# Performance work log

Measured on AMD Instinct MI355X. Metric: run time of the kernel, lower is better.

## Reference

```python
import jax, jax.numpy as jnp
import numpy as np

HIDDEN = 2048
N_HEADS = 32
N_KV = 8
HEAD_DIM = HIDDEN // N_HEADS
SEQ = 2048
BATCH = 1
THETA = 10000.0
EPS = 1e-5


def _layernorm(x, g, b):
    mu = jnp.mean(x, axis=-1, keepdims=True)
    var = jnp.var(x, axis=-1, keepdims=True)
    return (x - mu) * jax.lax.rsqrt(var + EPS) * g + b


def _rope_tables(seq_len, dim, theta):
    inv_freq = 1.0 / (theta ** (jnp.arange(0, dim, 2, dtype=jnp.float32) / dim))
    t = jnp.arange(seq_len, dtype=jnp.float32)
    freqs = jnp.einsum('i,j->ij', t, inv_freq)          # [S, D/2]
    emb = jnp.concatenate([freqs, freqs], axis=-1)       # [S, D]
    return jnp.cos(emb), jnp.sin(emb)


def _rotate_half(x):
    x1, x2 = jnp.split(x, 2, axis=-1)
    return jnp.concatenate([-x2, x1], axis=-1)


def setup_inputs() -> dict:
    key = jax.random.key(0)
    ks = jax.random.split(key, 10)
    s = 0.02
    return {
        'x':   jax.random.normal(ks[0], (BATCH, SEQ, HIDDEN), jnp.float32),
        'Wq':  jax.random.normal(ks[1], (HIDDEN, HIDDEN), jnp.float32) * s,
        'bq':  jnp.zeros((HIDDEN,), jnp.float32),
        'Wk':  jax.random.normal(ks[2], (HIDDEN, N_KV * HEAD_DIM), jnp.float32) * s,
        'bk':  jnp.zeros((N_KV * HEAD_DIM,), jnp.float32),
        'Wv':  jax.random.normal(ks[3], (HIDDEN, N_KV * HEAD_DIM), jnp.float32) * s,
        'bv':  jnp.zeros((N_KV * HEAD_DIM,), jnp.float32),
        'Wo':  jax.random.normal(ks[4], (HIDDEN, HIDDEN), jnp.float32) * s,
        'bo':  jnp.zeros((HIDDEN,), jnp.float32),
        'q_g': jnp.ones((HEAD_DIM,), jnp.float32),
        'q_b': jnp.zeros((HEAD_DIM,), jnp.float32),
        'k_g': jnp.ones((HEAD_DIM,), jnp.float32),
        'k_b': jnp.zeros((HEAD_DIM,), jnp.float32),
    }


def reference(x, Wq, bq, Wk, bk, Wv, bv, Wo, bo, q_g, q_b, k_g, k_b):
    B, S, H = x.shape
    n_rep = N_HEADS // N_KV
    # projections
    q = (x @ Wq + bq).reshape(B, S, N_HEADS, HEAD_DIM).transpose(0, 2, 1, 3)  # [B,Hq,S,D]
    k = (x @ Wk + bk).reshape(B, S, N_KV, HEAD_DIM).transpose(0, 2, 1, 3)     # [B,Hkv,S,D]
    v = (x @ Wv + bv).reshape(B, S, N_KV, HEAD_DIM).transpose(0, 2, 1, 3)
    # per-head QK layernorm
    q = _layernorm(q, q_g, q_b)
    k = _layernorm(k, k_g, k_b)
    # RoPE
    cos, sin = _rope_tables(S, HEAD_DIM, THETA)  # [S, D]
    q = q * cos + _rotate_half(q) * sin
    k = k * cos + _rotate_half(k) * sin
    # GQA attention without materializing repeated k/v:
    # repeat_interleave groups adjacent q-heads per kv head -> reshape q to [B,Hkv,rep,S,D]
    qg = q.reshape(B, N_KV, n_rep, S, HEAD_DIM)
    scores = jnp.einsum('bgrqd,bgkd->bgrqk', qg, k) / jnp.sqrt(jnp.float32(HEAD_DIM))
    attn = jax.nn.softmax(scores, axis=-1)
    out = jnp.einsum('bgrqk,bgkd->bgrqd', attn, v)  # [B,Hkv,rep,S,D]
    out = out.reshape(B, N_HEADS, S, HEAD_DIM).transpose(0, 2, 1, 3).reshape(B, S, H)
    return out @ Wo + bo
```

## Files before the change

### kernel.cpp

```cpp
#include <hip/hip_runtime.h>
#include <hip/hip_bf16.h>
#include <stdint.h>

#define S_LEN 2048
#define HID   2048
#define NH    32
#define NKV   8
#define HD    64

typedef __attribute__((ext_vector_type(8))) short bf16x8;
typedef __attribute__((ext_vector_type(4))) float f32x4;
typedef __attribute__((ext_vector_type(16))) float f32x16;

__device__ __forceinline__ short f2bf(float f) {
  __hip_bfloat16 h = __float2bfloat16(f);
  return __builtin_bit_cast(short, h);
}
__device__ __forceinline__ float bf2f(short s) {
  unsigned u = ((unsigned)(unsigned short)s) << 16;
  return __builtin_bit_cast(float, u);
}
__device__ __forceinline__ int cvt_pk_bf16(float lo, float hi) {
  int r;
  asm("v_cvt_pk_bf16_f32 %0, %1, %2" : "=v"(r) : "v"(lo), "v"(hi));
  return r;
}

__global__ void cast_bf16_kernel(const float* __restrict__ in, short* __restrict__ out, int n4) {
  int i = blockIdx.x * blockDim.x + threadIdx.x;
  if (i < n4) {
    float4 v = reinterpret_cast<const float4*>(in)[i];
    short4 o;
    o.x = f2bf(v.x); o.y = f2bf(v.y); o.z = f2bf(v.z); o.w = f2bf(v.w);
    reinterpret_cast<short4*>(out)[i] = o;
  }
}

__global__ void transpose_cast_kernel(const float* __restrict__ in, short* __restrict__ out,
                                      int K, int N) {
  __shared__ float tile[64][65];
  const int k0 = blockIdx.x * 64;
  const int n0 = blockIdx.y * 64;
  const int tn = threadIdx.x & 63;
  const int t4 = threadIdx.x >> 6;
#pragma unroll
  for (int i = 0; i < 16; i++)
    tile[t4 + i * 4][tn] = in[(size_t)(k0 + t4 + i * 4) * N + n0 + tn];
  __syncthreads();
#pragma unroll
  for (int i = 0; i < 16; i++)
    out[(size_t)(n0 + t4 + i * 4) * K + k0 + tn] = f2bf(tile[tn][t4 + i * 4]);
}

__global__ void concat_bias_kernel(const float* __restrict__ bq, const float* __restrict__ bk,
                                   const float* __restrict__ bv, float* __restrict__ out) {
  int i = blockIdx.x * blockDim.x + threadIdx.x;
  if (i < 3072) {
    float v = (i < 2048) ? bq[i] : (i < 2560 ? bk[i - 2048] : bv[i - 2560]);
    out[i] = v;
  }
}

__global__ void rope_table_kernel(float* __restrict__ ctab, float* __restrict__ stab) {
  int i = blockIdx.x * blockDim.x + threadIdx.x;
  if (i < S_LEN * 32) {
    int t = i >> 5, j = i & 31;
    float ang = (float)t * powf(10000.0f, -(float)j / 32.0f);
    ctab[i] = cosf(ang);
    stab[i] = sinf(ang);
  }
}

template <int F32OUT>
__global__ __launch_bounds__(256, 3) void gemm_v2_kernel(
    const short* __restrict__ A, const short* __restrict__ Bt,
    const float* __restrict__ bias, void* __restrict__ Cv,
    int N, int K) {
  __shared__ short Als[2][64 * 64];
  __shared__ short Bls[2][128 * 64];
  const int tid = threadIdx.x;
  const int l = tid & 63, w = tid >> 6;
  const int lg = l >> 4, lc = l & 15;
  const int wr = w >> 1, wc = w & 1;

  const int nwg = gridDim.x;
  const int cpx = nwg >> 3;
  const int swz = (blockIdx.x & 7) * cpx + (blockIdx.x >> 3);
  const int m0 = (swz & 31) << 6;
  const int n0 = (swz >> 5) << 7;

  const int NT = K >> 6;
  const f32x4 zero4 = {0.f, 0.f, 0.f, 0.f};
  f32x4 acc[2][4];
#pragma unroll
  for (int i = 0; i < 2; i++)
#pragma unroll
    for (int j = 0; j < 4; j++) acc[i][j] = zero4;

  const int lrow = l >> 3;
  const int lcol = (l & 7) << 3;

  auto stage = [&](int buf, int kt) {
    const int kofs = kt << 6;
#pragma unroll
    for (int i = 0; i < 2; i++) {
      const short* gsrc = A + (size_t)(m0 + i * 32 + (w << 3) + lrow) * K + kofs + lcol;
      __builtin_amdgcn_global_load_lds(
          (const __attribute__((address_space(1))) unsigned*)gsrc,
          (__attribute__((address_space(3))) unsigned*)(&Als[buf][(i * 32 + (w << 3)) << 6]),
          16, 0, 0);
    }
#pragma unroll
    for (int i = 0; i < 4; i++) {
      const short* gsrc = Bt + (size_t)(n0 + i * 32 + (w << 3) + lrow) * K + kofs + lcol;
      __builtin_amdgcn_global_load_lds(
          (const __attribute__((address_space(1))) unsigned*)gsrc,
          (__attribute__((address_space(3))) unsigned*)(&Bls[buf][(i * 32 + (w << 3)) << 6]),
          16, 0, 0);
    }
  };

  stage(0, 0);
  int cur = 0;
  for (int kt = 0; kt < NT; kt++) {
    __syncthreads();
    if (kt + 1 < NT) stage(cur ^ 1, kt + 1);
    const char* AB = reinterpret_cast<const char*>(Als[cur]);
    const char* BB = reinterpret_cast<const char*>(Bls[cur]);
#pragma unroll
    for (int ks = 0; ks < 2; ks++) {
      bf16x8 af[2], bfr[4];
#pragma unroll
      for (int mi = 0; mi < 2; mi++)
        af[mi] = *reinterpret_cast<const bf16x8*>(
            AB + (wr * 32 + mi * 16 + lc) * 128 + ks * 64 + lg * 16);
#pragma unroll
      for (int nf = 0; nf < 4; nf++)
        bfr[nf] = *reinterpret_cast<const bf16x8*>(
            BB + (wc * 64 + nf * 16 + lc) * 128 + ks * 64 + lg * 16);
#pragma unroll
      for (int mi = 0; mi < 2; mi++)
#pragma unroll
        for (int nf = 0; nf < 4; nf++)
          acc[mi][nf] = __builtin_amdgcn_mfma_f32_16x16x32_bf16(af[mi], bfr[nf], acc[mi][nf], 0, 0, 0);
    }
    cur ^= 1;
  }

#pragma unroll
  for (int mi = 0; mi < 2; mi++) {
#pragma unroll
    for (int nf = 0; nf < 4; nf++) {
      int col = n0 + wc * 64 + nf * 16 + lc;
      float bv = bias[col];
#pragma unroll
      for (int r = 0; r < 4; r++) {
        int rowg = m0 + wr * 32 + mi * 16 + lg * 4 + r;
        float v = acc[mi][nf][r] + bv;
        if (F32OUT)
          reinterpret_cast<float*>(Cv)[(size_t)rowg * N + col] = v;
        else
          reinterpret_cast<short*>(Cv)[(size_t)rowg * N + col] = f2bf(v);
      }
    }
  }
}

__global__ void ln_rope_kernel(const short* __restrict__ In, int instride, int nh_shift,
                               const float* __restrict__ gam, const float* __restrict__ bet,
                               const float* __restrict__ ctab, const float* __restrict__ stab,
                               float scale, short* __restrict__ Out) {
  const int lane = threadIdx.x & 63;
  const int nh = 1 << nh_shift;
  const int nrows = S_LEN << nh_shift;
  int row = (blockIdx.x * blockDim.x + threadIdx.x) >> 6;
  const int step = (gridDim.x * blockDim.x) >> 6;
  const float g = gam[lane], b = bet[lane];
  for (; row < nrows; row += step) {
    const int t = row >> nh_shift;
    const int h = row & (nh - 1);
    float x = bf2f(In[(size_t)t * instride + h * HD + lane]);
    float s = x;
#pragma unroll
    for (int m = 32; m >= 1; m >>= 1) s += __shfl_xor(s, m);
    const float mu = s * (1.0f / 64.0f);
    float d = x - mu;
    float v2 = d * d;
#pragma unroll
    for (int m = 32; m >= 1; m >>= 1) v2 += __shfl_xor(v2, m);
    const float var = v2 * (1.0f / 64.0f);
    float y = d * rsqrtf(var + 1e-5f) * g + b;
    float part = __shfl_xor(y, 32);
    const float c = ctab[t * 32 + (lane & 31)];
    const float sn = stab[t * 32 + (lane & 31)];
    float o = (lane < 32) ? (y * c - part * sn) : (y * c + part * sn);
    Out[((size_t)h * S_LEN + t) * HD + lane] = f2bf(o * scale);
  }
}

__global__ void v_transpose_kernel(const short* __restrict__ In, short* __restrict__ Vt) {
  __shared__ short tile[64][66];
  const int g = blockIdx.x;
  const int t0 = blockIdx.y * 64;
  const int lane = threadIdx.x & 63, w = threadIdx.x >> 6;
#pragma unroll
  for (int i = 0; i < 16; i++) {
    int r = i * 4 + w;
    tile[r][lane] = In[(size_t)(t0 + r) * 3072 + g * 64 + lane];
  }
  __syncthreads();
#pragma unroll
  for (int i = 0; i < 16; i++) {
    int d = i * 4 + w;
    Vt[((size_t)g * 64 + d) * 2048 + t0 + lane] = tile[lane][d];
  }
}

__global__ __launch_bounds__(256, 2) void attn_kernel(
    const short* __restrict__ Q, const short* __restrict__ Kk,
    const short* __restrict__ Vt, short* __restrict__ AO) {
  __shared__ short Kls[64 * 64];
  __shared__ short Vls[64 * 64];
  const int tid = threadIdx.x;
  const int l = tid & 63;
  const int w = tid >> 6;
  const int q31 = l & 31;
  const int h = l >> 5;

  const int v = (blockIdx.x & 7) * 32 + (blockIdx.x >> 3);
  const int g = v >> 5;
  const int within = v & 31;
  const int head = (g << 2) + (within >> 3);
  const int q0 = (within & 7) * 256 + w * 64;

  bf16x8 qf[2][4];
#pragma unroll
  for (int qb = 0; qb < 2; qb++) {
    const short* qbp = Q + ((size_t)head * S_LEN + q0 + qb * 32 + q31) * HD;
#pragma unroll
    for (int ks = 0; ks < 4; ks++)
      qf[qb][ks] = *reinterpret_cast<const bf16x8*>(qbp + ks * 16 + h * 8);
  }

  f32x16 oacc[2][2];
#pragma unroll
  for (int qb = 0; qb < 2; qb++)
#pragma unroll
    for (int df = 0; df < 2; df++)
#pragma unroll
      for (int r = 0; r < 16; r++) oacc[qb][df][r] = 0.f;
  float l_run[2] = {0.f, 0.f};

  const int srow = tid >> 3;
  const int kb = (tid & 7) << 4;
  const int kbs = kb ^ ((srow & 7) << 4);
  int4 kr[2], vr[2];
  auto stage_load = [&](int kt) {
#pragma unroll
    for (int c = 0; c < 2; c++) {
      int row = c * 32 + srow;
      kr[c] = *reinterpret_cast<const int4*>(Kk + ((size_t)g * S_LEN + kt * 64 + row) * HD + (kb >> 1));
      vr[c] = *reinterpret_cast<const int4*>(Vt + ((size_t)g * HD + row) * S_LEN + kt * 64 + (kb >> 1));
    }
  };
  stage_load(0);

  const int swz = (l & 7) << 4;
  const char* KB = reinterpret_cast<const char*>(Kls);
  const char* VB = reinterpret_cast<const char*>(Vls);

  for (int kt = 0; kt < S_LEN / 64; kt++) {
    __syncthreads();
#pragma unroll
    for (int c = 0; c < 2; c++) {
      int row = c * 32 + srow;
      *reinterpret_cast<int4*>(reinterpret_cast<char*>(Kls) + row * 128 + kbs) = kr[c];
      *reinterpret_cast<int4*>(reinterpret_cast<char*>(Vls) + row * 128 + kbs) = vr[c];
    }
    if (kt + 1 < S_LEN / 64) stage_load(kt + 1);
    __syncthreads();

    f32x16 sc0[2], sc1[2];
#pragma unroll
    for (int i = 0; i < 16; i++) { sc0[0][i] = 0.f; sc0[1][i] = 0.f; sc1[0][i] = 0.f; sc1[1][i] = 0.f; }
    __builtin_amdgcn_s_setprio(1);
#pragma unroll
    for (int ks = 0; ks < 4; ks++) {
#pragma unroll
      for (int kc = 0; kc < 2; kc++) {
        int row = kc * 32 + q31;
        bf16x8 kf = *reinterpret_cast<const bf16x8*>(KB + row * 128 + ((ks * 32 + h * 16) ^ swz));
        sc0[kc] = __builtin_amdgcn_mfma_f32_32x32x16_bf16(kf, qf[0][ks], sc0[kc], 0, 0, 0);
        sc1[kc] = __builtin_amdgcn_mfma_f32_32x32x16_bf16(kf, qf[1][ks], sc1[kc], 0, 0, 0);
      }
    }
    __builtin_amdgcn_s_setprio(0);

    bf16x8 pa[2][4];
#pragma unroll
    for (int qb = 0; qb < 2; qb++) {
      f32x16* sc = (qb == 0) ? sc0 : sc1;
      float ps = 0.f;
#pragma unroll
      for (int kc = 0; kc < 2; kc++)
#pragma unroll
        for (int r = 0; r < 16; r++) {
          float p = __builtin_exp2f(sc[kc][r] - 12.0f);
          sc[kc][r] = p;
          ps += p;
        }
      ps += __shfl_xor(ps, 32);
      l_run[qb] += ps;

#pragma unroll
      for (int c = 0; c < 4; c++) {
        const int b0 = (c & 1) * 8;
        int wa = cvt_pk_bf16(sc[c >> 1][b0 + 0], sc[c >> 1][b0 + 1]);
        int wb = cvt_pk_bf16(sc[c >> 1][b0 + 4], sc[c >> 1][b0 + 5]);
        asm volatile("v_permlane32_swap_b32 %0, %1" : "+v"(wa), "+v"(wb));
        int wc2 = cvt_pk_bf16(sc[c >> 1][b0 + 2], sc[c >> 1][b0 + 3]);
        int wd = cvt_pk_bf16(sc[c >> 1][b0 + 6], sc[c >> 1][b0 + 7]);
        asm volatile("v_permlane32_swap_b32 %0, %1" : "+v"(wc2), "+v"(wd));
        int4 pw;
        pw.x = wa; pw.y = wc2; pw.z = wb; pw.w = wd;
        pa[qb][c] = __builtin_bit_cast(bf16x8, pw);
      }
    }

    __builtin_amdgcn_s_setprio(1);
#pragma unroll
    for (int df = 0; df < 2; df++) {
#pragma unroll
      for (int c = 0; c < 4; c++) {
        int row = df * 32 + q31;
        bf16x8 vf = *reinterpret_cast<const bf16x8*>(VB + row * 128 + ((c * 32 + h * 16) ^ swz));
        oacc[0][df] = __builtin_amdgcn_mfma_f32_32x32x16_bf16(vf, pa[0][c], oacc[0][df], 0, 0, 0);
        oacc[1][df] = __builtin_amdgcn_mfma_f32_32x32x16_bf16(vf, pa[1][c], oacc[1][df], 0, 0, 0);
      }
    }
    __builtin_amdgcn_s_setprio(0);
  }

#pragma unroll
  for (int qb = 0; qb < 2; qb++) {
    float inv = 1.0f / l_run[qb];
    short* aob = AO + (size_t)(q0 + qb * 32 + q31) * HID + head * HD;
#pragma unroll
    for (int df = 0; df < 2; df++) {
#pragma unroll
      for (int rq = 0; rq < 4; rq++) {
        int v0 = cvt_pk_bf16(oacc[qb][df][rq * 4 + 0] * inv, oacc[qb][df][rq * 4 + 1] * inv);
        int v1 = cvt_pk_bf16(oacc[qb][df][rq * 4 + 2] * inv, oacc[qb][df][rq * 4 + 3] * inv);
        int2 st;
        st.x = v0; st.y = v1;
        *reinterpret_cast<int2*>(aob + df * 32 + rq * 8 + h * 4) = st;
      }
    }
  }
}

extern "C" void kernel_launch(void* const* d_in, const int* in_sizes, int n_in,
                              void* d_out, int out_size, void* d_ws, size_t ws_size,
                              hipStream_t stream) {
  const float* x  = (const float*)d_in[0];
  const float* Wq = (const float*)d_in[1];
  const float* bq = (const float*)d_in[2];
  const float* Wk = (const float*)d_in[3];
  const float* bk = (const float*)d_in[4];
  const float* Wv = (const float*)d_in[5];
  const float* bv = (const float*)d_in[6];
  const float* Wo = (const float*)d_in[7];
  const float* bo = (const float*)d_in[8];
  const float* qg = (const float*)d_in[9];
  const float* qb = (const float*)d_in[10];
  const float* kg = (const float*)d_in[11];
  const float* kb2 = (const float*)d_in[12];
  float* out = (float*)d_out;

  char* ws = (char*)d_ws;
  size_t off = 0;
  auto alloc = [&](size_t bytes) {
    void* p = ws + off;
    off += (bytes + 255) & ~(size_t)255;
    return p;
  };
  short* xb    = (short*)alloc((size_t)2048 * 2048 * 2);
  short* Wqkvt = (short*)alloc((size_t)3072 * 2048 * 2);
  short* Wot   = (short*)alloc((size_t)2048 * 2048 * 2);
  short* QKVp  = (short*)alloc((size_t)2048 * 3072 * 2);
  short* Qr    = (short*)alloc((size_t)NH * 2048 * 64 * 2);
  short* Kr    = (short*)alloc((size_t)NKV * 2048 * 64 * 2);
  short* Vt    = (short*)alloc((size_t)NKV * 64 * 2048 * 2);
  short* AO    = (short*)alloc((size_t)2048 * 2048 * 2);
  float* ctab  = (float*)alloc((size_t)2048 * 32 * 4);
  float* stab  = (float*)alloc((size_t)2048 * 32 * 4);
  float* bqkv  = (float*)alloc((size_t)3072 * 4);

  cast_bf16_kernel<<<(2048 * 2048 / 4 + 255) / 256, 256, 0, stream>>>(x, xb, 2048 * 2048 / 4);
  transpose_cast_kernel<<<dim3(32, 32), 256, 0, stream>>>(Wq, Wqkvt, 2048, 2048);
  transpose_cast_kernel<<<dim3(32, 8), 256, 0, stream>>>(Wk, Wqkvt + (size_t)2048 * 2048, 2048, 512);
  transpose_cast_kernel<<<dim3(32, 8), 256, 0, stream>>>(Wv, Wqkvt + (size_t)2560 * 2048, 2048, 512);
  transpose_cast_kernel<<<dim3(32, 32), 256, 0, stream>>>(Wo, Wot, 2048, 2048);
  concat_bias_kernel<<<12, 256, 0, stream>>>(bq, bk, bv, bqkv);
  rope_table_kernel<<<256, 256, 0, stream>>>(ctab, stab);

  gemm_v2_kernel<0><<<768, 256, 0, stream>>>(xb, Wqkvt, bqkv, QKVp, 3072, 2048);

  ln_rope_kernel<<<512, 256, 0, stream>>>(QKVp, 3072, 5, qg, qb, ctab, stab, 0.125f * 1.44269504089f, Qr);
  ln_rope_kernel<<<256, 256, 0, stream>>>(QKVp + 2048, 3072, 3, kg, kb2, ctab, stab, 1.0f, Kr);
  v_transpose_kernel<<<dim3(8, 32), 256, 0, stream>>>(QKVp + 2560, Vt);

  attn_kernel<<<256, 256, 0, stream>>>(Qr, Kr, Vt, AO);

  gemm_v2_kernel<1><<<512, 256, 0, stream>>>(AO, Wot, bo, out, 2048, 2048);
}
```

Before: 344.6 us.

## Split attention KV range in two and merge partial outputs in combine kernel

The attention grid doubles from 256 to 512 blocks, and each block handles half of the key sequence. Each block writes an unnormalized bf16 partial output plus its row sums. A new combine kernel adds the two partials and divides by the summed normalizers. The goal is to fill two blocks per CU for better latency hiding. The costs are an extra launch, extra memory traffic for the partials, and some bf16 rounding of unnormalized sums. The split is valid only because the softmax keeps no running max.

```diff
diff --git a/kernel.cpp b/kernel.cpp
--- a/kernel.cpp
+++ b/kernel.cpp
@@ -218,7 +218,8 @@
 
 __global__ __launch_bounds__(256, 2) void attn_kernel(
     const short* __restrict__ Q, const short* __restrict__ Kk,
-    const short* __restrict__ Vt, short* __restrict__ AO) {
+    const short* __restrict__ Vt, short* __restrict__ Op0,
+    short* __restrict__ Op1, float* __restrict__ lpart) {
   __shared__ short Kls[64 * 64];
   __shared__ short Vls[64 * 64];
   const int tid = threadIdx.x;
@@ -227,11 +228,17 @@
   const int q31 = l & 31;
   const int h = l >> 5;
 
-  const int v = (blockIdx.x & 7) * 32 + (blockIdx.x >> 3);
+  const int bid = blockIdx.x;
+  const int sp = bid >> 8;
+  const int id8 = bid & 255;
+  const int v = (id8 & 7) * 32 + (id8 >> 3);
   const int g = v >> 5;
   const int within = v & 31;
   const int head = (g << 2) + (within >> 3);
   const int q0 = (within & 7) * 256 + w * 64;
+
+  short* __restrict__ Op = sp ? Op1 : Op0;
+  float* __restrict__ lp = lpart + sp * (NH * S_LEN);
 
   bf16x8 qf[2][4];
 #pragma unroll
@@ -263,13 +270,15 @@
       vr[c] = *reinterpret_cast<const int4*>(Vt + ((size_t)g * HD + row) * S_LEN + kt * 64 + (kb >> 1));
     }
   };
-  stage_load(0);
+
+  const int kt0 = sp << 4, kt1 = kt0 + 16;
+  stage_load(kt0);
 
   const int swz = (l & 7) << 4;
   const char* KB = reinterpret_cast<const char*>(Kls);
   const char* VB = reinterpret_cast<const char*>(Vls);
 
-  for (int kt = 0; kt < S_LEN / 64; kt++) {
+  for (int kt = kt0; kt < kt1; kt++) {
     __syncthreads();
 #pragma unroll
     for (int c = 0; c < 2; c++) {
@@ -277,7 +286,7 @@
       *reinterpret_cast<int4*>(reinterpret_cast<char*>(Kls) + row * 128 + kbs) = kr[c];
       *reinterpret_cast<int4*>(reinterpret_cast<char*>(Vls) + row * 128 + kbs) = vr[c];
     }
-    if (kt + 1 < S_LEN / 64) stage_load(kt + 1);
+    if (kt + 1 < kt1) stage_load(kt + 1);
     __syncthreads();
 
     f32x16 sc0[2], sc1[2];
@@ -343,20 +352,37 @@
 
 #pragma unroll
   for (int qb = 0; qb < 2; qb++) {
-    float inv = 1.0f / l_run[qb];
-    short* aob = AO + (size_t)(q0 + qb * 32 + q31) * HID + head * HD;
+    const int q = q0 + qb * 32 + q31;
+    if (h == 0) lp[head * S_LEN + q] = l_run[qb];
+    short* ob = Op + (size_t)q * HID + head * HD;
 #pragma unroll
     for (int df = 0; df < 2; df++) {
 #pragma unroll
       for (int rq = 0; rq < 4; rq++) {
-        int v0 = cvt_pk_bf16(oacc[qb][df][rq * 4 + 0] * inv, oacc[qb][df][rq * 4 + 1] * inv);
-        int v1 = cvt_pk_bf16(oacc[qb][df][rq * 4 + 2] * inv, oacc[qb][df][rq * 4 + 3] * inv);
+        int v0 = cvt_pk_bf16(oacc[qb][df][rq * 4 + 0], oacc[qb][df][rq * 4 + 1]);
+        int v1 = cvt_pk_bf16(oacc[qb][df][rq * 4 + 2], oacc[qb][df][rq * 4 + 3]);
         int2 st;
         st.x = v0; st.y = v1;
-        *reinterpret_cast<int2*>(aob + df * 32 + rq * 8 + h * 4) = st;
+        *reinterpret_cast<int2*>(ob + df * 32 + rq * 8 + h * 4) = st;
       }
     }
   }
+}
+
+__global__ void combine_kernel(const short* __restrict__ Op0, const short* __restrict__ Op1,
+                               const float* __restrict__ lpart, short* __restrict__ AO) {
+  int i = blockIdx.x * blockDim.x + threadIdx.x;
+  int t = i >> 9;
+  int c = i & 511;
+  int h = c >> 4;
+  float inv = 1.0f / (lpart[h * S_LEN + t] + lpart[NH * S_LEN + h * S_LEN + t]);
+  short4 a = reinterpret_cast<const short4*>(Op0)[i];
+  short4 b = reinterpret_cast<const short4*>(Op1)[i];
+  int v0 = cvt_pk_bf16((bf2f(a.x) + bf2f(b.x)) * inv, (bf2f(a.y) + bf2f(b.y)) * inv);
+  int v1 = cvt_pk_bf16((bf2f(a.z) + bf2f(b.z)) * inv, (bf2f(a.w) + bf2f(b.w)) * inv);
+  int2 st;
+  st.x = v0; st.y = v1;
+  reinterpret_cast<int2*>(AO)[i] = st;
 }
 
 extern "C" void kernel_launch(void* const* d_in, const int* in_sizes, int n_in,
@@ -395,6 +421,9 @@
   float* ctab  = (float*)alloc((size_t)2048 * 32 * 4);
   float* stab  = (float*)alloc((size_t)2048 * 32 * 4);
   float* bqkv  = (float*)alloc((size_t)3072 * 4);
+  float* lpart = (float*)alloc((size_t)2 * NH * 2048 * 4);
+  short* Op0 = QKVp;
+  short* Op1 = xb;
 
   cast_bf16_kernel<<<(2048 * 2048 / 4 + 255) / 256, 256, 0, stream>>>(x, xb, 2048 * 2048 / 4);
   transpose_cast_kernel<<<dim3(32, 32), 256, 0, stream>>>(Wq, Wqkvt, 2048, 2048);
@@ -410,7 +439,8 @@
   ln_rope_kernel<<<256, 256, 0, stream>>>(QKVp + 2048, 3072, 3, kg, kb2, ctab, stab, 1.0f, Kr);
   v_transpose_kernel<<<dim3(8, 32), 256, 0, stream>>>(QKVp + 2560, Vt);
 
-  attn_kernel<<<256, 256, 0, stream>>>(Qr, Kr, Vt, AO);
+  attn_kernel<<<512, 256, 0, stream>>>(Qr, Kr, Vt, Op0, Op1, lpart);
+  combine_kernel<<<4096, 256, 0, stream>>>(Op0, Op1, lpart, AO);
 
   gemm_v2_kernel<1><<<512, 256, 0, stream>>>(AO, Wot, bo, out, 2048, 2048);
 }
```

New measurement: 329.8 us. -4.3%, faster.
